# Performance work log

Measured on AMD Instinct MI355X. Metric: run time of the kernel, lower is better.

The kernel has to match this reference:

```python
import jax, jax.numpy as jnp
import numpy as np

T, D, DI, E, K = 8192, 512, 256, 8, 2  # tokens, in_features, d_intermediate, n_routed_experts, top_k


def setup_inputs() -> dict:
    key = jax.random.key(0)
    k1, k2, k3, k4 = jax.random.split(key, 4)
    x = jax.random.normal(k1, (T, D), jnp.float32)
    # Gate linear weight (nn.Linear(in_features, n_routed_experts, bias=False))
    wg = jax.random.normal(k2, (E, D), jnp.float32) / np.sqrt(D).astype(np.float32)
    # fc1: [E, 2*d_intermediate, in_features] / sqrt(in_features)
    fc1 = jax.random.normal(k3, (E, 2 * DI, D), jnp.float32) / np.sqrt(D).astype(np.float32)
    # fc2: [E, in_features, d_intermediate] / sqrt(d_intermediate)
    fc2 = jax.random.normal(k4, (E, D, DI), jnp.float32) / np.sqrt(DI).astype(np.float32)
    return {"x": x, "wg": wg, "fc1": fc1, "fc2": fc2}


def reference(x, wg, fc1, fc2):
    route_scale = 1.0
    T_, D_ = x.shape
    E_ = fc1.shape[0]
    # --- Gate: softmax scores -> top-k routing weights / expert indices ---
    scores = jax.nn.softmax(x @ wg.T, axis=-1)            # [T, E]
    weights, indices = jax.lax.top_k(scores, K)           # [T, K]
    weights = weights * route_scale
    # --- Routed experts: per (token, activated-expert) pair ---
    idx_flat = indices.reshape(-1)                        # [T*K] expert id per pair
    x_pairs = jnp.repeat(x, K, axis=0)                    # [T*K, D] (pair p -> token p//K)
    out_pairs = jnp.zeros_like(x_pairs)
    for e in range(E_):                                   # fixed small expert loop
        h = x_pairs @ fc1[e].T                            # [T*K, 2*DI]
        y, gate = jnp.split(h, 2, axis=-1)                # chunk(2, dim=-1)
        o = (y * jax.nn.silu(gate)) @ fc2[e].T            # [T*K, D]
        out_pairs = out_pairs + jnp.where((idx_flat == e)[:, None], o, 0.0)
    # combine: z[t] = sum_k weights[t,k] * out_pairs[t,k]  (torch.bmm(weights[:,None], x_by_expert))
    z = jnp.einsum('tk,tkd->td', weights, out_pairs.reshape(T_, K, D_))
    return z
```

## Files before the change

kernel.cpp:

```cpp
#include <hip/hip_runtime.h>
#include <hip/hip_bf16.h>
#include <stdint.h>

#define T_TOK 8192
#define D_IN  512
#define DINT  256
#define NE    8

typedef float f32x4 __attribute__((ext_vector_type(4)));
typedef short bf16x8 __attribute__((ext_vector_type(8)));
typedef unsigned short u16;
typedef unsigned short u16x4 __attribute__((ext_vector_type(4)));

#define WS_CNT   0
#define WS_WP    1024
#define WS_BT    66560
#define WS_F2B   197632
#define WS_F1B   2294784
#define WS_XB    6489088
#define WS_AS    14877696
#define WS_OG    23725056

typedef const __attribute__((address_space(1))) void* gptr_t;
typedef __attribute__((address_space(3))) void* lptr_t;
#define GLL16(g, s) __builtin_amdgcn_global_load_lds((gptr_t)(g), (lptr_t)(s), 16, 0, 0)

static __device__ __forceinline__ u16 f32_bf16(float f) {
    union { float f; uint32_t u; } v; v.f = f;
    uint32_t u = v.u;
    uint32_t r = (u + 0x7FFFu + ((u >> 16) & 1u)) >> 16;
    return (u16)r;
}
static __device__ __forceinline__ float bf16_f32(u16 h) {
    union { uint32_t u; float f; } v; v.u = ((uint32_t)h) << 16; return v.f;
}

__global__ __launch_bounds__(256) void cvt_kernel(
    const float* __restrict__ fc1, const float* __restrict__ fc2,
    u16* __restrict__ f1s, u16* __restrict__ f2s, int* __restrict__ cnt)
{
    if (blockIdx.x == 0 && threadIdx.x < NE) cnt[threadIdx.x] = 0;
    const int C1 = NE * 4 * 16 * 512;
    const int C2 = NE * 4 * 8 * 512;
    for (int c = blockIdx.x * 256 + threadIdx.x; c < C1 + C2; c += gridDim.x * 256) {
        const float* s; u16* d;
        if (c < C1) {
            int lane = c & 63, f = (c >> 6) & 7, ks = (c >> 9) & 15, p = c >> 13;
            int e = p >> 2, nt = p & 3;
            int row = ((f < 4) ? (nt * 64 + f * 16) : (256 + nt * 64 + (f - 4) * 16)) + (lane & 15);
            int k = ks * 32 + (lane >> 4) * 8;
            s = fc1 + (size_t)e * 512 * 512 + (size_t)row * 512 + k;
            d = f1s + (size_t)c * 8;
        } else {
            int c2 = c - C1;
            int lane = c2 & 63, f = (c2 >> 6) & 7, ks = (c2 >> 9) & 7, p = c2 >> 12;
            int e = p >> 2, nt = p & 3;
            int row = nt * 128 + f * 16 + (lane & 15);
            int k = ks * 32 + (lane >> 4) * 8;
            s = fc2 + (size_t)e * 512 * 256 + (size_t)row * 256 + k;
            d = f2s + (size_t)c2 * 8;
        }
        float4 v0 = *(const float4*)s;
        float4 v1 = *(const float4*)(s + 4);
        bf16x8 o;
        o[0] = (short)f32_bf16(v0.x); o[1] = (short)f32_bf16(v0.y);
        o[2] = (short)f32_bf16(v0.z); o[3] = (short)f32_bf16(v0.w);
        o[4] = (short)f32_bf16(v1.x); o[5] = (short)f32_bf16(v1.y);
        o[6] = (short)f32_bf16(v1.z); o[7] = (short)f32_bf16(v1.w);
        *(bf16x8*)d = o;
    }
}

__global__ __launch_bounds__(256) void gate_kernel(
    const float* __restrict__ x, const float* __restrict__ wg,
    int* __restrict__ cnt, u16* __restrict__ bt, float* __restrict__ wpair,
    u16* __restrict__ xb)
{
    __shared__ float wgl[NE * D_IN];
    __shared__ float xt[256][33];
    __shared__ float part[256 * 9];
    __shared__ int ecnt[NE];
    __shared__ int gbase[NE];

    const int tid = threadIdx.x;
    const int t0  = blockIdx.x * 32;
    const int tl  = tid & 31;
    const int kq  = tid >> 5;

    for (int i = tid; i < NE * D_IN; i += 256) wgl[i] = wg[i];
    if (tid < NE) ecnt[tid] = 0;

    float acc[NE];
#pragma unroll
    for (int e = 0; e < NE; e++) acc[e] = 0.f;

    for (int c = 0; c < 2; ++c) {
        __syncthreads();
#pragma unroll
        for (int i = 0; i < 8; ++i) {
            int idx = i * 256 + tid;
            int row = idx >> 6, c4 = idx & 63;
            float4 v = *(const float4*)&x[(size_t)(t0 + row) * D_IN + c * 256 + c4 * 4];
            u16x4 o;
            o.x = f32_bf16(v.x); o.y = f32_bf16(v.y);
            o.z = f32_bf16(v.z); o.w = f32_bf16(v.w);
            *(u16x4*)&xb[(size_t)(t0 + row) * D_IN + c * 256 + c4 * 4] = o;
            xt[c4 * 4 + 0][row] = v.x; xt[c4 * 4 + 1][row] = v.y;
            xt[c4 * 4 + 2][row] = v.z; xt[c4 * 4 + 3][row] = v.w;
        }
        __syncthreads();
#pragma unroll
        for (int j = 0; j < 32; ++j) {
            float xv = xt[kq * 32 + j][tl];
#pragma unroll
            for (int e = 0; e < NE; e++)
                acc[e] = fmaf(xv, wgl[e * D_IN + c * 256 + kq * 32 + j], acc[e]);
        }
    }
#pragma unroll
    for (int e = 0; e < NE; e++) part[tid * 9 + e] = acc[e];
    __syncthreads();

    int i1 = 0, i2 = -1, lp1 = 0, lp2 = 0;
    if (tid < 32) {
        float s8[NE];
#pragma unroll
        for (int e = 0; e < NE; e++) {
            float s = 0.f;
#pragma unroll
            for (int q = 0; q < 8; q++) s += part[(q * 32 + tid) * 9 + e];
            s8[e] = s;
        }
        float m = s8[0];
#pragma unroll
        for (int e = 1; e < NE; e++) m = fmaxf(m, s8[e]);
        float p[NE], s = 0.f;
#pragma unroll
        for (int e = 0; e < NE; e++) { p[e] = expf(s8[e] - m); s += p[e]; }
        float inv = 1.f / s;
        float v1 = p[0];
#pragma unroll
        for (int e = 1; e < NE; e++) if (p[e] > v1) { v1 = p[e]; i1 = e; }
        float v2 = -1.f;
#pragma unroll
        for (int e = 0; e < NE; e++) if (e != i1 && p[e] > v2) { v2 = p[e]; i2 = e; }
        int t = t0 + tid;
        wpair[2 * t]     = v1 * inv;
        wpair[2 * t + 1] = v2 * inv;
        lp1 = atomicAdd(&ecnt[i1], 1);
        lp2 = atomicAdd(&ecnt[i2], 1);
    }
    __syncthreads();
    if (tid < NE) gbase[tid] = atomicAdd(&cnt[tid], ecnt[tid]);
    __syncthreads();
    if (tid < 32) {
        int t = t0 + tid;
        bt[i1 * T_TOK + gbase[i1] + lp1] = (u16)(2 * t);
        bt[i2 * T_TOK + gbase[i2] + lp2] = (u16)(2 * t + 1);
    }
}

__global__ __launch_bounds__(256) void fc1_kernel(
    const u16* __restrict__ xb, const u16* __restrict__ f1s,
    const int* __restrict__ cnt, const u16* __restrict__ bt,
    u16* __restrict__ acts)
{
    __shared__ __align__(16) u16 asl[3][4096];
    __shared__ __align__(16) u16 bsl[3][4096];
    __shared__ u16 slot_l[128];

    const int bid = blockIdx.x;
    const int e   = bid & 7;
    const int nt  = (bid >> 3) & 3;
    const int mt  = bid >> 5;
    const int n   = cnt[e];
    const int row0 = mt * 128;
    if (row0 >= n) return;

    int tpre = 0;
#pragma unroll
    for (int ee = 0; ee < NE; ++ee)
        if (ee < e) tpre += (cnt[ee] + 127) >> 7;

    const int tid = threadIdx.x;
    const int wv  = tid >> 6, lane = tid & 63;
    const int l15 = lane & 15, lhi = lane >> 4;
    const int wr  = wv >> 1, wc = wv & 1;

    if (tid < 128) {
        int r = row0 + tid;
        slot_l[tid] = bt[e * T_TOK + ((r < n) ? r : (n - 1))];
    }
    __syncthreads();

    const u16* srcA0 = xb + (size_t)(slot_l[(wv * 2 + 0) * 16 + l15] >> 1) * D_IN + lhi * 8;
    const u16* srcA1 = xb + (size_t)(slot_l[(wv * 2 + 1) * 16 + l15] >> 1) * D_IN + lhi * 8;
    const int fb0 = wv * 2, fb1 = wv * 2 + 1;
    const u16* srcB0 = f1s + (size_t)(e * 4 + nt) * 65536 + fb0 * 512 + lane * 8;
    const u16* srcB1 = f1s + (size_t)(e * 4 + nt) * 65536 + fb1 * 512 + lane * 8;

#define ISS1(KS, BUF) {                                          \
    GLL16(srcA0 + (KS) * 32,   &asl[BUF][fb0 * 512]);            \
    GLL16(srcA1 + (KS) * 32,   &asl[BUF][fb1 * 512]);            \
    GLL16(srcB0 + (KS) * 4096, &bsl[BUF][fb0 * 512]);            \
    GLL16(srcB1 + (KS) * 4096, &bsl[BUF][fb1 * 512]); }

    f32x4 acc[4][4];
#pragma unroll
    for (int m = 0; m < 4; m++)
#pragma unroll
        for (int nb = 0; nb < 4; nb++) acc[m][nb] = (f32x4)0.f;

    ISS1(0, 0);
    ISS1(1, 1);
    asm volatile("s_waitcnt vmcnt(4)" ::: "memory");
    __builtin_amdgcn_s_barrier();

#pragma unroll
    for (int ks = 0; ks < 16; ++ks) {
        const int cur = ks % 3;
        if (ks + 2 < 16) ISS1(ks + 2, (ks + 2) % 3);
        bf16x8 a[4], b[4];
#pragma unroll
        for (int m = 0; m < 4; m++)
            a[m] = *(const bf16x8*)&asl[cur][(wr * 4 + m) * 512 + lane * 8];
        b[0] = *(const bf16x8*)&bsl[cur][(wc * 2 + 0) * 512 + lane * 8];
        b[1] = *(const bf16x8*)&bsl[cur][(wc * 2 + 1) * 512 + lane * 8];
        b[2] = *(const bf16x8*)&bsl[cur][(4 + wc * 2 + 0) * 512 + lane * 8];
        b[3] = *(const bf16x8*)&bsl[cur][(4 + wc * 2 + 1) * 512 + lane * 8];
#pragma unroll
        for (int m = 0; m < 4; m++)
#pragma unroll
            for (int nb = 0; nb < 4; nb++)
                acc[m][nb] = __builtin_amdgcn_mfma_f32_16x16x32_bf16(
                    a[m], b[nb], acc[m][nb], 0, 0, 0);
        if (ks < 15) {
            if (ks + 2 < 16) asm volatile("s_waitcnt vmcnt(4)" ::: "memory");
            else             asm volatile("s_waitcnt vmcnt(0)" ::: "memory");
            __builtin_amdgcn_s_barrier();
        }
    }
    __syncthreads();

    u16* glu = &asl[0][0];
#pragma unroll
    for (int m = 0; m < 4; m++) {
#pragma unroll
        for (int j = 0; j < 4; j++) {
            int row = wr * 64 + m * 16 + lhi * 4 + j;
#pragma unroll
            for (int q = 0; q < 2; q++) {
                float y = acc[m][q][j], gv = acc[m][q + 2][j];
                float v = y * gv / (1.f + __expf(-gv));
                glu[row * 72 + wc * 32 + q * 16 + l15] = f32_bf16(v);
            }
        }
    }
    __syncthreads();

    u16* tile = acts + (size_t)(tpre + mt) * 32768;
#pragma unroll
    for (int i = 0; i < 4; ++i) {
        int c = wv * 4 + i;
        int mf = c >> 1, ksr = c & 1;
        bf16x8 v = *(const bf16x8*)&glu[(mf * 16 + l15) * 72 + ksr * 32 + lhi * 8];
        *(bf16x8*)&tile[(2 * nt + ksr) * 4096 + mf * 512 + lane * 8] = v;
    }
#undef ISS1
}

__global__ __launch_bounds__(256) void fc2_kernel(
    const u16* __restrict__ acts, const u16* __restrict__ f2s,
    const int* __restrict__ cnt, const u16* __restrict__ bt,
    u16* __restrict__ og)
{
    __shared__ __align__(16) u16 asl[3][4096];
    __shared__ __align__(16) u16 bsl[3][4096];
    __shared__ u16 slot_l[128];

    const int bid = blockIdx.x;
    const int e   = bid & 7;
    const int nt  = (bid >> 3) & 3;
    const int mt  = bid >> 5;
    const int n   = cnt[e];
    const int row0 = mt * 128;
    if (row0 >= n) return;

    int tpre = 0;
#pragma unroll
    for (int ee = 0; ee < NE; ++ee)
        if (ee < e) tpre += (cnt[ee] + 127) >> 7;

    const int tid = threadIdx.x;
    const int wv  = tid >> 6, lane = tid & 63;
    const int l15 = lane & 15, lhi = lane >> 4;
    const int wr  = wv >> 1, wc = wv & 1;

    if (tid < 128) {
        int r = row0 + tid;
        slot_l[tid] = bt[e * T_TOK + ((r < n) ? r : (n - 1))];
    }
    __syncthreads();

    const int fb0 = wv * 2, fb1 = wv * 2 + 1;
    const u16* srcA0 = acts + (size_t)(tpre + mt) * 32768 + fb0 * 512 + lane * 8;
    const u16* srcA1 = acts + (size_t)(tpre + mt) * 32768 + fb1 * 512 + lane * 8;
    const u16* srcB0 = f2s + (size_t)(e * 4 + nt) * 32768 + fb0 * 512 + lane * 8;
    const u16* srcB1 = f2s + (size_t)(e * 4 + nt) * 32768 + fb1 * 512 + lane * 8;

#define ISS2(KS, BUF) {                                          \
    GLL16(srcA0 + (KS) * 4096, &asl[BUF][fb0 * 512]);            \
    GLL16(srcA1 + (KS) * 4096, &asl[BUF][fb1 * 512]);            \
    GLL16(srcB0 + (KS) * 4096, &bsl[BUF][fb0 * 512]);            \
    GLL16(srcB1 + (KS) * 4096, &bsl[BUF][fb1 * 512]); }

    f32x4 acc[4][4];
#pragma unroll
    for (int m = 0; m < 4; m++)
#pragma unroll
        for (int nb = 0; nb < 4; nb++) acc[m][nb] = (f32x4)0.f;

    ISS2(0, 0);
    ISS2(1, 1);
    asm volatile("s_waitcnt vmcnt(4)" ::: "memory");
    __builtin_amdgcn_s_barrier();

#pragma unroll
    for (int ks = 0; ks < 8; ++ks) {
        const int cur = ks % 3;
        if (ks + 2 < 8) ISS2(ks + 2, (ks + 2) % 3);
        bf16x8 a[4], b[4];
#pragma unroll
        for (int m = 0; m < 4; m++)
            a[m] = *(const bf16x8*)&asl[cur][(wr * 4 + m) * 512 + lane * 8];
#pragma unroll
        for (int nb = 0; nb < 4; nb++)
            b[nb] = *(const bf16x8*)&bsl[cur][(wc * 4 + nb) * 512 + lane * 8];
#pragma unroll
        for (int m = 0; m < 4; m++)
#pragma unroll
            for (int nb = 0; nb < 4; nb++)
                acc[m][nb] = __builtin_amdgcn_mfma_f32_16x16x32_bf16(
                    a[m], b[nb], acc[m][nb], 0, 0, 0);
        if (ks < 7) {
            if (ks + 2 < 8) asm volatile("s_waitcnt vmcnt(4)" ::: "memory");
            else            asm volatile("s_waitcnt vmcnt(0)" ::: "memory");
            __builtin_amdgcn_s_barrier();
        }
    }

#pragma unroll
    for (int m = 0; m < 4; m++) {
#pragma unroll
        for (int j = 0; j < 4; j++) {
            int lrow = wr * 64 + m * 16 + lhi * 4 + j;
            if (row0 + lrow < n) {
                int slot = slot_l[lrow];
                u16* dst = og + (size_t)slot * D_IN + nt * 128 + wc * 64 + l15;
#pragma unroll
                for (int nb = 0; nb < 4; nb++)
                    dst[nb * 16] = f32_bf16(acc[m][nb][j]);
            }
        }
    }
#undef ISS2
}

__global__ __launch_bounds__(256) void combine_kernel(
    const u16* __restrict__ og, const float* __restrict__ wpair,
    float* __restrict__ out)
{
    int idx = blockIdx.x * 256 + threadIdx.x;
    int t  = idx >> 6;
    int c8 = (idx & 63) * 8;
    float w0 = wpair[2 * t], w1 = wpair[2 * t + 1];
    bf16x8 a = *(const bf16x8*)&og[(size_t)(2 * t) * D_IN + c8];
    bf16x8 b = *(const bf16x8*)&og[(size_t)(2 * t + 1) * D_IN + c8];
    float4 o0, o1;
#pragma unroll
    for (int j = 0; j < 4; j++) {
        o0[j] = w0 * bf16_f32((u16)a[j])     + w1 * bf16_f32((u16)b[j]);
        o1[j] = w0 * bf16_f32((u16)a[j + 4]) + w1 * bf16_f32((u16)b[j + 4]);
    }
    float* orow = out + (size_t)t * D_IN + c8;
    *(float4*)orow = o0;
    *(float4*)(orow + 4) = o1;
}

extern "C" void kernel_launch(void* const* d_in, const int* in_sizes, int n_in,
                              void* d_out, int out_size, void* d_ws, size_t ws_size,
                              hipStream_t stream) {
    const float* x   = (const float*)d_in[0];
    const float* wg  = (const float*)d_in[1];
    const float* fc1 = (const float*)d_in[2];
    const float* fc2 = (const float*)d_in[3];
    float* out = (float*)d_out;
    char* ws = (char*)d_ws;

    int*   cnt   = (int*)(ws + WS_CNT);
    float* wpair = (float*)(ws + WS_WP);
    u16*   bt    = (u16*)(ws + WS_BT);
    u16*   f2s   = (u16*)(ws + WS_F2B);
    u16*   f1s   = (u16*)(ws + WS_F1B);
    u16*   xb    = (u16*)(ws + WS_XB);
    u16*   acts  = (u16*)(ws + WS_AS);
    u16*   og    = (u16*)(ws + WS_OG);

    cvt_kernel<<<1024, 256, 0, stream>>>(fc1, fc2, f1s, f2s, cnt);
    gate_kernel<<<T_TOK / 32, 256, 0, stream>>>(x, wg, cnt, bt, wpair, xb);
    fc1_kernel<<<2048, 256, 0, stream>>>(xb, f1s, cnt, bt, acts);
    fc2_kernel<<<2048, 256, 0, stream>>>(acts, f2s, cnt, bt, og);
    combine_kernel<<<T_TOK * (D_IN / 8) / 256, 256, 0, stream>>>(og, wpair, out);
}
```

Measured before the change: 66.77 us.

## Halve expert GEMM M-tile to 64 rows with double-buffered pipeline

Cuts the row tile of the fc1 and fc2 grouped GEMMs from 128 to 64 tokens, doubles the grid, and keeps the 128-row activation tile layout by having each block write or read one half of it. The three-stage LDS pipeline with vmcnt-based waits becomes a simpler two-buffer scheme with a full barrier every k-step. The aim is more blocks and higher occupancy, and less wasted padding on the last tile of each expert. The cost is half the MFMA work per B load, so weight traffic doubles, and a shallower prefetch pipeline.

Measured after the change: 66.07 us. No clear change (-1.1%).

```diff
diff --git a/kernel.cpp b/kernel.cpp
--- a/kernel.cpp
+++ b/kernel.cpp
@@ -165,89 +165,82 @@
     const int* __restrict__ cnt, const u16* __restrict__ bt,
     u16* __restrict__ acts)
 {
-    __shared__ __align__(16) u16 asl[3][4096];
-    __shared__ __align__(16) u16 bsl[3][4096];
-    __shared__ u16 slot_l[128];
+    __shared__ __align__(16) u16 asl[2][2048];
+    __shared__ __align__(16) u16 bsl[2][4096];
+    __shared__ u16 slot_l[64];
 
     const int bid = blockIdx.x;
     const int e   = bid & 7;
     const int nt  = (bid >> 3) & 3;
     const int mt  = bid >> 5;
     const int n   = cnt[e];
-    const int row0 = mt * 128;
+    const int row0 = mt * 64;
     if (row0 >= n) return;
 
     int tpre = 0;
 #pragma unroll
     for (int ee = 0; ee < NE; ++ee)
         if (ee < e) tpre += (cnt[ee] + 127) >> 7;
+    const int g = tpre + (mt >> 1);
+    const int mhalf = mt & 1;
 
     const int tid = threadIdx.x;
     const int wv  = tid >> 6, lane = tid & 63;
     const int l15 = lane & 15, lhi = lane >> 4;
     const int wr  = wv >> 1, wc = wv & 1;
 
-    if (tid < 128) {
+    if (tid < 64) {
         int r = row0 + tid;
         slot_l[tid] = bt[e * T_TOK + ((r < n) ? r : (n - 1))];
     }
     __syncthreads();
 
-    const u16* srcA0 = xb + (size_t)(slot_l[(wv * 2 + 0) * 16 + l15] >> 1) * D_IN + lhi * 8;
-    const u16* srcA1 = xb + (size_t)(slot_l[(wv * 2 + 1) * 16 + l15] >> 1) * D_IN + lhi * 8;
+    const u16* srcA  = xb + (size_t)(slot_l[wv * 16 + l15] >> 1) * D_IN + lhi * 8;
     const int fb0 = wv * 2, fb1 = wv * 2 + 1;
     const u16* srcB0 = f1s + (size_t)(e * 4 + nt) * 65536 + fb0 * 512 + lane * 8;
     const u16* srcB1 = f1s + (size_t)(e * 4 + nt) * 65536 + fb1 * 512 + lane * 8;
 
 #define ISS1(KS, BUF) {                                          \
-    GLL16(srcA0 + (KS) * 32,   &asl[BUF][fb0 * 512]);            \
-    GLL16(srcA1 + (KS) * 32,   &asl[BUF][fb1 * 512]);            \
+    GLL16(srcA  + (KS) * 32,   &asl[BUF][wv * 512]);             \
     GLL16(srcB0 + (KS) * 4096, &bsl[BUF][fb0 * 512]);            \
     GLL16(srcB1 + (KS) * 4096, &bsl[BUF][fb1 * 512]); }
 
-    f32x4 acc[4][4];
-#pragma unroll
-    for (int m = 0; m < 4; m++)
+    f32x4 acc[2][4];
+#pragma unroll
+    for (int m = 0; m < 2; m++)
 #pragma unroll
         for (int nb = 0; nb < 4; nb++) acc[m][nb] = (f32x4)0.f;
 
     ISS1(0, 0);
-    ISS1(1, 1);
-    asm volatile("s_waitcnt vmcnt(4)" ::: "memory");
-    __builtin_amdgcn_s_barrier();
+    __syncthreads();
 
 #pragma unroll
     for (int ks = 0; ks < 16; ++ks) {
-        const int cur = ks % 3;
-        if (ks + 2 < 16) ISS1(ks + 2, (ks + 2) % 3);
-        bf16x8 a[4], b[4];
-#pragma unroll
-        for (int m = 0; m < 4; m++)
-            a[m] = *(const bf16x8*)&asl[cur][(wr * 4 + m) * 512 + lane * 8];
+        const int cur = ks & 1;
+        if (ks < 15) ISS1(ks + 1, cur ^ 1);
+        bf16x8 a[2], b[4];
+#pragma unroll
+        for (int m = 0; m < 2; m++)
+            a[m] = *(const bf16x8*)&asl[cur][(wr * 2 + m) * 512 + lane * 8];
         b[0] = *(const bf16x8*)&bsl[cur][(wc * 2 + 0) * 512 + lane * 8];
         b[1] = *(const bf16x8*)&bsl[cur][(wc * 2 + 1) * 512 + lane * 8];
         b[2] = *(const bf16x8*)&bsl[cur][(4 + wc * 2 + 0) * 512 + lane * 8];
         b[3] = *(const bf16x8*)&bsl[cur][(4 + wc * 2 + 1) * 512 + lane * 8];
 #pragma unroll
-        for (int m = 0; m < 4; m++)
+        for (int m = 0; m < 2; m++)
 #pragma unroll
             for (int nb = 0; nb < 4; nb++)
                 acc[m][nb] = __builtin_amdgcn_mfma_f32_16x16x32_bf16(
                     a[m], b[nb], acc[m][nb], 0, 0, 0);
-        if (ks < 15) {
-            if (ks + 2 < 16) asm volatile("s_waitcnt vmcnt(4)" ::: "memory");
-            else             asm volatile("s_waitcnt vmcnt(0)" ::: "memory");
-            __builtin_amdgcn_s_barrier();
-        }
-    }
-    __syncthreads();
-
-    u16* glu = &asl[0][0];
-#pragma unroll
-    for (int m = 0; m < 4; m++) {
+        __syncthreads();
+    }
+
+    u16* glu = &bsl[0][0];
+#pragma unroll
+    for (int m = 0; m < 2; m++) {
 #pragma unroll
         for (int j = 0; j < 4; j++) {
-            int row = wr * 64 + m * 16 + lhi * 4 + j;
+            int row = wr * 32 + m * 16 + lhi * 4 + j;
 #pragma unroll
             for (int q = 0; q < 2; q++) {
                 float y = acc[m][q][j], gv = acc[m][q + 2][j];
@@ -258,13 +251,13 @@
     }
     __syncthreads();
 
-    u16* tile = acts + (size_t)(tpre + mt) * 32768;
-#pragma unroll
-    for (int i = 0; i < 4; ++i) {
-        int c = wv * 4 + i;
-        int mf = c >> 1, ksr = c & 1;
-        bf16x8 v = *(const bf16x8*)&glu[(mf * 16 + l15) * 72 + ksr * 32 + lhi * 8];
-        *(bf16x8*)&tile[(2 * nt + ksr) * 4096 + mf * 512 + lane * 8] = v;
+    u16* tile = acts + (size_t)g * 32768;
+#pragma unroll
+    for (int i = 0; i < 2; ++i) {
+        int c = wv * 2 + i;
+        int mfl = c >> 1, ksr = c & 1;
+        bf16x8 v = *(const bf16x8*)&glu[(mfl * 16 + l15) * 72 + ksr * 32 + lhi * 8];
+        *(bf16x8*)&tile[(2 * nt + ksr) * 4096 + (mhalf * 4 + mfl) * 512 + lane * 8] = v;
     }
 #undef ISS1
 }
@@ -274,86 +267,80 @@
     const int* __restrict__ cnt, const u16* __restrict__ bt,
     u16* __restrict__ og)
 {
-    __shared__ __align__(16) u16 asl[3][4096];
-    __shared__ __align__(16) u16 bsl[3][4096];
-    __shared__ u16 slot_l[128];
+    __shared__ __align__(16) u16 asl[2][2048];
+    __shared__ __align__(16) u16 bsl[2][4096];
+    __shared__ u16 slot_l[64];
 
     const int bid = blockIdx.x;
     const int e   = bid & 7;
     const int nt  = (bid >> 3) & 3;
     const int mt  = bid >> 5;
     const int n   = cnt[e];
-    const int row0 = mt * 128;
+    const int row0 = mt * 64;
     if (row0 >= n) return;
 
     int tpre = 0;
 #pragma unroll
     for (int ee = 0; ee < NE; ++ee)
         if (ee < e) tpre += (cnt[ee] + 127) >> 7;
+    const int g = tpre + (mt >> 1);
+    const int mhalf = mt & 1;
 
     const int tid = threadIdx.x;
     const int wv  = tid >> 6, lane = tid & 63;
     const int l15 = lane & 15, lhi = lane >> 4;
     const int wr  = wv >> 1, wc = wv & 1;
 
-    if (tid < 128) {
+    if (tid < 64) {
         int r = row0 + tid;
         slot_l[tid] = bt[e * T_TOK + ((r < n) ? r : (n - 1))];
     }
     __syncthreads();
 
     const int fb0 = wv * 2, fb1 = wv * 2 + 1;
-    const u16* srcA0 = acts + (size_t)(tpre + mt) * 32768 + fb0 * 512 + lane * 8;
-    const u16* srcA1 = acts + (size_t)(tpre + mt) * 32768 + fb1 * 512 + lane * 8;
+    const u16* srcA  = acts + (size_t)g * 32768 + (mhalf * 4 + wv) * 512 + lane * 8;
     const u16* srcB0 = f2s + (size_t)(e * 4 + nt) * 32768 + fb0 * 512 + lane * 8;
     const u16* srcB1 = f2s + (size_t)(e * 4 + nt) * 32768 + fb1 * 512 + lane * 8;
 
 #define ISS2(KS, BUF) {                                          \
-    GLL16(srcA0 + (KS) * 4096, &asl[BUF][fb0 * 512]);            \
-    GLL16(srcA1 + (KS) * 4096, &asl[BUF][fb1 * 512]);            \
+    GLL16(srcA  + (KS) * 4096, &asl[BUF][wv * 512]);             \
     GLL16(srcB0 + (KS) * 4096, &bsl[BUF][fb0 * 512]);            \
     GLL16(srcB1 + (KS) * 4096, &bsl[BUF][fb1 * 512]); }
 
-    f32x4 acc[4][4];
-#pragma unroll
-    for (int m = 0; m < 4; m++)
+    f32x4 acc[2][4];
+#pragma unroll
+    for (int m = 0; m < 2; m++)
 #pragma unroll
         for (int nb = 0; nb < 4; nb++) acc[m][nb] = (f32x4)0.f;
 
     ISS2(0, 0);
-    ISS2(1, 1);
-    asm volatile("s_waitcnt vmcnt(4)" ::: "memory");
-    __builtin_amdgcn_s_barrier();
+    __syncthreads();
 
 #pragma unroll
     for (int ks = 0; ks < 8; ++ks) {
-        const int cur = ks % 3;
-        if (ks + 2 < 8) ISS2(ks + 2, (ks + 2) % 3);
-        bf16x8 a[4], b[4];
-#pragma unroll
-        for (int m = 0; m < 4; m++)
-            a[m] = *(const bf16x8*)&asl[cur][(wr * 4 + m) * 512 + lane * 8];
+        const int cur = ks & 1;
+        if (ks < 7) ISS2(ks + 1, cur ^ 1);
+        bf16x8 a[2], b[4];
+#pragma unroll
+        for (int m = 0; m < 2; m++)
+            a[m] = *(const bf16x8*)&asl[cur][(wr * 2 + m) * 512 + lane * 8];
 #pragma unroll
         for (int nb = 0; nb < 4; nb++)
             b[nb] = *(const bf16x8*)&bsl[cur][(wc * 4 + nb) * 512 + lane * 8];
 #pragma unroll
-        for (int m = 0; m < 4; m++)
+        for (int m = 0; m < 2; m++)
 #pragma unroll
             for (int nb = 0; nb < 4; nb++)
                 acc[m][nb] = __builtin_amdgcn_mfma_f32_16x16x32_bf16(
                     a[m], b[nb], acc[m][nb], 0, 0, 0);
-        if (ks < 7) {
-            if (ks + 2 < 8) asm volatile("s_waitcnt vmcnt(4)" ::: "memory");
-            else            asm volatile("s_waitcnt vmcnt(0)" ::: "memory");
-            __builtin_amdgcn_s_barrier();
-        }
-    }
-
-#pragma unroll
-    for (int m = 0; m < 4; m++) {
+        __syncthreads();
+    }
+
+#pragma unroll
+    for (int m = 0; m < 2; m++) {
 #pragma unroll
         for (int j = 0; j < 4; j++) {
-            int lrow = wr * 64 + m * 16 + lhi * 4 + j;
+            int lrow = wr * 32 + m * 16 + lhi * 4 + j;
             if (row0 + lrow < n) {
                 int slot = slot_l[lrow];
                 u16* dst = og + (size_t)slot * D_IN + nt * 128 + wc * 64 + l15;
@@ -408,7 +395,7 @@
 
     cvt_kernel<<<1024, 256, 0, stream>>>(fc1, fc2, f1s, f2s, cnt);
     gate_kernel<<<T_TOK / 32, 256, 0, stream>>>(x, wg, cnt, bt, wpair, xb);
-    fc1_kernel<<<2048, 256, 0, stream>>>(xb, f1s, cnt, bt, acts);
-    fc2_kernel<<<2048, 256, 0, stream>>>(acts, f2s, cnt, bt, og);
+    fc1_kernel<<<4096, 256, 0, stream>>>(xb, f1s, cnt, bt, acts);
+    fc2_kernel<<<4096, 256, 0, stream>>>(acts, f2s, cnt, bt, og);
     combine_kernel<<<T_TOK * (D_IN / 8) / 256, 256, 0, stream>>>(og, wpair, out);
 }
```
